# Optimization experiments

Hardware: AMD Instinct MI355X
Metric: run time of the kernel (lower is better)

Reference implementation:

```python
import jax, jax.numpy as jnp
import numpy as np

POOL = (2, 2)
B, H, W, C = 8, 128, 128, 256
FLAT_OUT = (H * POOL[0]) * (W * POOL[1]) * C  # 16,777,216


def setup_inputs() -> dict:
    key = jax.random.key(0)
    k1, k2 = jax.random.split(key)
    updates = jax.random.normal(k1, (B, H, W, C), dtype=jnp.float32)
    mask = jax.random.randint(k2, (B, H, W, C), 0, FLAT_OUT, dtype=jnp.int32)
    return {"updates": updates, "mask": mask}


def reference(updates, mask):
    ph, pw = POOL
    b, h, w, c = updates.shape
    hout, wout = h * ph, w * pw
    flat_input_size = h * w * c            # NOTE: original uses INPUT size as batch offset
    flat_output_size = hout * wout * c
    # per-batch offset (replicates b * flat_input_size from the TF code)
    batch_range = jnp.arange(b, dtype=jnp.int32).reshape(-1, 1, 1, 1)
    flat_mask = (mask.astype(jnp.int32) + batch_range * flat_input_size).reshape(-1)
    flat_updates = updates.reshape(-1)
    flat_output = jnp.zeros((b * flat_output_size,), dtype=updates.dtype)
    flat_output = flat_output.at[flat_mask].add(flat_updates)
    return flat_output.reshape(b, hout, wout, c)
```

## Files before the change

kernel.cpp:

```cpp
#include <hip/hip_runtime.h>


typedef float floatx4 __attribute__((ext_vector_type(4)));

constexpr int FLAT_IN   = 1 << 22;
constexpr int N_ELEMS   = 8 * FLAT_IN;
constexpr int OUT_WIN   = 7 * FLAT_IN + (1 << 24);
constexpr int OUT_TOTAL = 134217728;

constexpr int FB_SHIFT = 14;
constexpr int BKT_SIZE = 1 << FB_SHIFT;
constexpr int NBF      = OUT_WIN >> FB_SHIFT;
constexpr int CB_SHIFT = 16;
constexpr int NBC      = OUT_WIN >> CB_SHIFT;
constexpr int NBC_PAD  = 768;

constexpr int PBLOCK   = 1024;
constexpr int CHUNK    = 131072;
constexpr int NBLK     = N_ELEMS / CHUNK;
constexpr int ITERS    = CHUNK / (4 * PBLOCK);
constexpr int SEGS     = 8;
constexpr int SEG_ROWS = NBLK / SEGS;

constexpr size_t WS_PAIRS  = 0;
constexpr size_t WS_HISTC  = 268435456;
constexpr size_t WS_SEGC   = WS_HISTC + (size_t)NBLK * NBC_PAD * 4;
constexpr size_t WS_BBC    = WS_SEGC + (size_t)SEGS * NBC_PAD * 4;
constexpr size_t WS_FH     = WS_BBC + 3328;
constexpr size_t WS_BBF    = WS_FH + (size_t)NBF * 4;
constexpr size_t WS_NEEDED = WS_BBF + (size_t)(NBF + 1) * 4;

__global__ __launch_bounds__(256) void zero_kernel(floatx4* __restrict__ p, int n4) {
  int i = blockIdx.x * 256 + threadIdx.x;
  int stride = gridDim.x * 256;
  floatx4 z = {0.f, 0.f, 0.f, 0.f};
  for (; i < n4; i += stride) __builtin_nontemporal_store(z, p + i);
}

__global__ __launch_bounds__(PBLOCK) void p1_hist(const int4* __restrict__ mask4,
                                                  int* __restrict__ hist_c,
                                                  int* __restrict__ fhist) {
  __shared__ int cnt[1024];
  const int blk = blockIdx.x, tid = threadIdx.x;
  if (tid < 1024) cnt[tid] = 0;
  __syncthreads();
  const int base4 = blk * (CHUNK / 4);
  #pragma unroll 4
  for (int k = 0; k < ITERS; ++k) {
    int4 m = mask4[base4 + k * PBLOCK + tid];
    atomicAdd(&cnt[m.x >> FB_SHIFT], 1);
    atomicAdd(&cnt[m.y >> FB_SHIFT], 1);
    atomicAdd(&cnt[m.z >> FB_SHIFT], 1);
    atomicAdd(&cnt[m.w >> FB_SHIFT], 1);
  }
  __syncthreads();
  const int boff = (blk * CHUNK) & ~(FLAT_IN - 1);
  const int f0   = boff >> FB_SHIFT;
  const int cb0  = f0 >> 2;
  for (int j = tid; j < 1024; j += PBLOCK)
    if (cnt[j]) atomicAdd(&fhist[f0 + j], cnt[j]);
  for (int j = tid; j < NBC_PAD; j += PBLOCK) {
    int v = 0;
    int jj = j - cb0;
    if (jj >= 0 && jj < 256)
      v = cnt[4 * jj] + cnt[4 * jj + 1] + cnt[4 * jj + 2] + cnt[4 * jj + 3];
    hist_c[blk * NBC_PAD + j] = v;
  }
}

__global__ __launch_bounds__(256) void p2_segsum(const int* __restrict__ hist,
                                                 int* __restrict__ segsum) {
  int b = blockIdx.x * 256 + threadIdx.x;
  int seg = blockIdx.y;
  const int* p = hist + (size_t)(seg * SEG_ROWS) * NBC_PAD + b;
  int s = 0;
  #pragma unroll 4
  for (int k = 0; k < SEG_ROWS; ++k) s += p[(size_t)k * NBC_PAD];
  segsum[seg * NBC_PAD + b] = s;
}

__global__ __launch_bounds__(256) void p2_scan_c(const int* __restrict__ segsum,
                                                 int* __restrict__ bbase) {
  __shared__ int tot[NBC_PAD];
  __shared__ int partial[256];
  const int t = threadIdx.x;
  for (int j = t; j < NBC_PAD; j += 256) {
    int s = 0;
    #pragma unroll
    for (int g = 0; g < SEGS; ++g) s += segsum[g * NBC_PAD + j];
    tot[j] = s;
  }
  __syncthreads();
  int local = 0;
  #pragma unroll
  for (int k = 0; k < NBC_PAD / 256; ++k) local += tot[t * (NBC_PAD / 256) + k];
  partial[t] = local;
  __syncthreads();
  for (int off = 1; off < 256; off <<= 1) {
    int tmp = (t >= off) ? partial[t - off] : 0;
    __syncthreads();
    partial[t] += tmp;
    __syncthreads();
  }
  int run = partial[t] - local;
  #pragma unroll
  for (int k = 0; k < NBC_PAD / 256; ++k) {
    int b = t * (NBC_PAD / 256) + k;
    bbase[b] = run;
    run += tot[b];
  }
  if (t == 255) bbase[NBC_PAD] = run;
}

__global__ __launch_bounds__(256) void p2_expand(int* __restrict__ hist,
                                                 const int* __restrict__ segsum) {
  int b = blockIdx.x * 256 + threadIdx.x;
  int seg = blockIdx.y;
  int run = 0;
  for (int g = 0; g < seg; ++g) run += segsum[g * NBC_PAD + b];
  int* p = hist + (size_t)(seg * SEG_ROWS) * NBC_PAD + b;
  for (int k = 0; k < SEG_ROWS; ++k) {
    int v = p[(size_t)k * NBC_PAD];
    p[(size_t)k * NBC_PAD] = run;
    run += v;
  }
}

__global__ __launch_bounds__(256) void p2_scan_f(const int* __restrict__ fhist,
                                                 int* __restrict__ bbase) {
  __shared__ int tot[NBF];
  __shared__ int partial[256];
  const int t = threadIdx.x;
  for (int j = t; j < NBF; j += 256) tot[j] = fhist[j];
  __syncthreads();
  int local = 0;
  #pragma unroll
  for (int k = 0; k < NBF / 256; ++k) local += tot[t * (NBF / 256) + k];
  partial[t] = local;
  __syncthreads();
  for (int off = 1; off < 256; off <<= 1) {
    int tmp = (t >= off) ? partial[t - off] : 0;
    __syncthreads();
    partial[t] += tmp;
    __syncthreads();
  }
  int run = partial[t] - local;
  #pragma unroll
  for (int k = 0; k < NBF / 256; ++k) {
    int b = t * (NBF / 256) + k;
    bbase[b] = run;
    run += tot[b];
  }
  if (t == 255) bbase[NBF] = run;
}

__global__ __launch_bounds__(PBLOCK) void p3a_place(const int4* __restrict__ mask4,
                                                    const float4* __restrict__ upd4,
                                                    const int* __restrict__ hist_c,
                                                    const int* __restrict__ bbase_c,
                                                    int2* __restrict__ pout) {
  __shared__ int cnt[256];
  __shared__ int rowbase[256];
  const int blk = blockIdx.x, tid = threadIdx.x;
  const int boff = (blk * CHUNK) & ~(FLAT_IN - 1);
  const int cb0 = boff >> CB_SHIFT;
  if (tid < 256) {
    cnt[tid] = 0;
    rowbase[tid] = bbase_c[cb0 + tid] + hist_c[blk * NBC_PAD + cb0 + tid];
  }
  __syncthreads();
  const int base4 = blk * (CHUNK / 4);
  #pragma unroll 2
  for (int k = 0; k < ITERS; ++k) {
    int j4 = base4 + k * PBLOCK + tid;
    int4 m = mask4[j4];
    float4 u = upd4[j4];
    {
      int b = m.x >> CB_SHIFT; int r = atomicAdd(&cnt[b], 1);
      pout[rowbase[b] + r] = make_int2(m.x + boff, __float_as_int(u.x));
    }
    {
      int b = m.y >> CB_SHIFT; int r = atomicAdd(&cnt[b], 1);
      pout[rowbase[b] + r] = make_int2(m.y + boff, __float_as_int(u.y));
    }
    {
      int b = m.z >> CB_SHIFT; int r = atomicAdd(&cnt[b], 1);
      pout[rowbase[b] + r] = make_int2(m.z + boff, __float_as_int(u.z));
    }
    {
      int b = m.w >> CB_SHIFT; int r = atomicAdd(&cnt[b], 1);
      pout[rowbase[b] + r] = make_int2(m.w + boff, __float_as_int(u.w));
    }
  }
}

__device__ __forceinline__ void pushA(int idx, int val, int* cnt, const int* fb,
                                      int2* __restrict__ pout) {
  int f = (idx >> FB_SHIFT) & 3;
  unsigned long long act = __ballot(1);
  unsigned long long b0 = __ballot(f & 1);
  unsigned long long b1 = __ballot(f & 2);
  unsigned long long mf = ((f & 1) ? b0 : ~b0) & ((f & 2) ? b1 : ~b1) & act;
  int lane = threadIdx.x & 63;
  int rank = __popcll(mf & ((1ull << lane) - 1ull));
  int leader = __ffsll((unsigned long long)mf) - 1;
  int r0 = 0;
  if (lane == leader) r0 = atomicAdd(&cnt[f], __popcll(mf));
  r0 = __shfl(r0, leader);
  pout[fb[f] + r0 + rank] = make_int2(idx, val);
}

__global__ __launch_bounds__(512) void p3b_fine(const int2* __restrict__ pin,
                                                const int* __restrict__ bbase_c,
                                                const int* __restrict__ bbase_f,
                                                int2* __restrict__ pout) {
  __shared__ int cnt[4];
  __shared__ int fb[4];
  const int cb = blockIdx.x, tid = threadIdx.x;
  if (tid < 4) {
    cnt[tid] = 0;
    fb[tid] = bbase_f[cb * 4 + tid];
  }
  __syncthreads();
  const int s = bbase_c[cb], e = bbase_c[cb + 1];
  const int s4 = (s + 1) & ~1;
  if ((s & 1) && s < e && tid == 0) {
    int2 p = pin[s];
    int f = (p.x >> FB_SHIFT) & 3;
    int r = atomicAdd(&cnt[f], 1);
    pout[fb[f] + r] = p;
  }
  const int n2 = (e > s4) ? ((e - s4) >> 1) : 0;
  const int4* pv = (const int4*)(pin + s4);
  for (int i = tid; i < n2; i += 512) {
    int4 q = pv[i];
    pushA(q.x, q.y, cnt, fb, pout);
    pushA(q.z, q.w, cnt, fb, pout);
  }
  if ((e > s4) && ((e - s4) & 1) && tid == 0) {
    int2 p = pin[e - 1];
    int f = (p.x >> FB_SHIFT) & 3;
    int r = atomicAdd(&cnt[f], 1);
    pout[fb[f] + r] = p;
  }
}

__global__ __launch_bounds__(256) void p4_apply(const int2* __restrict__ pairs,
                                                const int* __restrict__ bbase,
                                                float* __restrict__ out) {
  __shared__ float win[BKT_SIZE];
  const int bkt = blockIdx.x, tid = threadIdx.x;
  floatx4* w4 = (floatx4*)win;
  floatx4 z = {0.f, 0.f, 0.f, 0.f};
  #pragma unroll
  for (int k = 0; k < BKT_SIZE / 1024; ++k) w4[k * 256 + tid] = z;
  __syncthreads();
  const int s = bbase[bkt], e = bbase[bkt + 1];
  const int s4 = (s + 1) & ~1;
  if ((s & 1) && s < e && tid == 0) {
    int2 p = pairs[s];
    atomicAdd(&win[p.x & (BKT_SIZE - 1)], __int_as_float(p.y));
  }
  const int n2 = (e > s4) ? ((e - s4) >> 1) : 0;
  const int4* pv = (const int4*)(pairs + s4);
  for (int i = tid; i < n2; i += 256) {
    int4 q = pv[i];
    atomicAdd(&win[q.x & (BKT_SIZE - 1)], __int_as_float(q.y));
    atomicAdd(&win[q.z & (BKT_SIZE - 1)], __int_as_float(q.w));
  }
  if ((e > s4) && ((e - s4) & 1) && tid == 0) {
    int2 p = pairs[e - 1];
    atomicAdd(&win[p.x & (BKT_SIZE - 1)], __int_as_float(p.y));
  }
  __syncthreads();
  floatx4* o4 = (floatx4*)(out + (size_t)bkt * BKT_SIZE);
  #pragma unroll
  for (int k = 0; k < BKT_SIZE / 1024; ++k)
    __builtin_nontemporal_store(w4[k * 256 + tid], o4 + k * 256 + tid);
}

__global__ __launch_bounds__(256) void scatter_add4_kernel(
    const float4* __restrict__ upd4, const int4* __restrict__ msk4,
    float* __restrict__ out, int n4) {
  int j = blockIdx.x * blockDim.x + threadIdx.x;
  if (j >= n4) return;
  float4 u = upd4[j];
  int4 m = msk4[j];
  int base = (j * 4) & ~(FLAT_IN - 1);
  unsafeAtomicAdd(out + (base + m.x), u.x);
  unsafeAtomicAdd(out + (base + m.y), u.y);
  unsafeAtomicAdd(out + (base + m.z), u.z);
  unsafeAtomicAdd(out + (base + m.w), u.w);
}

extern "C" void kernel_launch(void* const* d_in, const int* in_sizes, int n_in,
                              void* d_out, int out_size, void* d_ws, size_t ws_size,
                              hipStream_t stream) {
  const float* updates = (const float*)d_in[0];
  const int*   mask    = (const int*)d_in[1];
  float*       out     = (float*)d_out;
  const int n = in_sizes[0];

  const bool fast = (n == N_ELEMS) && (out_size == OUT_TOTAL) && (ws_size >= WS_NEEDED);

  if (!fast) {
    int n4z = out_size / 4;
    zero_kernel<<<(n4z + 2047) / 2048, 256, 0, stream>>>((floatx4*)d_out, n4z);
    int n4 = n / 4;
    scatter_add4_kernel<<<(n4 + 255) / 256, 256, 0, stream>>>(
        (const float4*)updates, (const int4*)mask, out, n4);
    return;
  }

  char* ws = (char*)d_ws;
  int2* pairs_f = (int2*)(ws + WS_PAIRS);
  int*  hist_c  = (int*)(ws + WS_HISTC);
  int*  segsum  = (int*)(ws + WS_SEGC);
  int*  bbase_c = (int*)(ws + WS_BBC);
  int*  fhist   = (int*)(ws + WS_FH);
  int*  bbase_f = (int*)(ws + WS_BBF);
  int2* pairs_c = (int2*)(out + OUT_WIN);

  zero_kernel<<<1, 256, 0, stream>>>((floatx4*)fhist, NBF / 4);
  p1_hist<<<NBLK, PBLOCK, 0, stream>>>((const int4*)mask, hist_c, fhist);
  p2_segsum<<<dim3(NBC_PAD / 256, SEGS), 256, 0, stream>>>(hist_c, segsum);
  p2_scan_c<<<1, 256, 0, stream>>>(segsum, bbase_c);
  p2_expand<<<dim3(NBC_PAD / 256, SEGS), 256, 0, stream>>>(hist_c, segsum);
  p2_scan_f<<<1, 256, 0, stream>>>(fhist, bbase_f);
  p3a_place<<<NBLK, PBLOCK, 0, stream>>>((const int4*)mask, (const float4*)updates,
                                         hist_c, bbase_c, pairs_c);
  p3b_fine<<<NBC, 512, 0, stream>>>(pairs_c, bbase_c, bbase_f, pairs_f);
  {
    int n4 = (OUT_TOTAL - OUT_WIN) / 4;
    zero_kernel<<<5376, 256, 0, stream>>>((floatx4*)(out + OUT_WIN), n4);
  }
  p4_apply<<<NBF, 256, 0, stream>>>(pairs_f, bbase_f, out);
}
```

Before: 1.219 ms.

## Drop fine bucketing pass; apply from coarse buckets with split 128KB LDS windows

Removes the fine histogram, its scan, and the second partitioning pass (p3b_fine) that re-sorted the pairs into 16K-element buckets. Pairs are now written once, into coarse 64K-element buckets in workspace. Each coarse bucket is then read by two blocks, and each block accumulates only the half that matches its selector bit into a 32K-float LDS window. The same apply kernel also zero-fills the output tail beyond the window, so the separate zero kernel goes away, and the block order is permuted. This saves one full read and write of the pair stream, at the cost of each coarse bucket's pairs being read twice and of larger 1024-thread blocks with 128KB of LDS, which may lower occupancy.

```diff
diff --git a/kernel.cpp b/kernel.cpp
--- a/kernel.cpp
+++ b/kernel.cpp
@@ -8,12 +8,14 @@
 constexpr int OUT_WIN   = 7 * FLAT_IN + (1 << 24);
 constexpr int OUT_TOTAL = 134217728;
 
-constexpr int FB_SHIFT = 14;
-constexpr int BKT_SIZE = 1 << FB_SHIFT;
-constexpr int NBF      = OUT_WIN >> FB_SHIFT;
 constexpr int CB_SHIFT = 16;
 constexpr int NBC      = OUT_WIN >> CB_SHIFT;
 constexpr int NBC_PAD  = 768;
+
+constexpr int AP_SHIFT = 15;
+constexpr int APW      = 1 << AP_SHIFT;
+constexpr int NAP      = OUT_TOTAL >> AP_SHIFT;
+constexpr int NAP_WIN  = OUT_WIN >> AP_SHIFT;
 
 constexpr int PBLOCK   = 1024;
 constexpr int CHUNK    = 131072;
@@ -26,9 +28,7 @@
 constexpr size_t WS_HISTC  = 268435456;
 constexpr size_t WS_SEGC   = WS_HISTC + (size_t)NBLK * NBC_PAD * 4;
 constexpr size_t WS_BBC    = WS_SEGC + (size_t)SEGS * NBC_PAD * 4;
-constexpr size_t WS_FH     = WS_BBC + 3328;
-constexpr size_t WS_BBF    = WS_FH + (size_t)NBF * 4;
-constexpr size_t WS_NEEDED = WS_BBF + (size_t)(NBF + 1) * 4;
+constexpr size_t WS_NEEDED = WS_BBC + (size_t)(NBC_PAD + 1) * 4;
 
 __global__ __launch_bounds__(256) void zero_kernel(floatx4* __restrict__ p, int n4) {
   int i = blockIdx.x * 256 + threadIdx.x;
@@ -38,33 +38,25 @@
 }
 
 __global__ __launch_bounds__(PBLOCK) void p1_hist(const int4* __restrict__ mask4,
-                                                  int* __restrict__ hist_c,
-                                                  int* __restrict__ fhist) {
-  __shared__ int cnt[1024];
+                                                  int* __restrict__ hist_c) {
+  __shared__ int cnt[256];
   const int blk = blockIdx.x, tid = threadIdx.x;
-  if (tid < 1024) cnt[tid] = 0;
+  if (tid < 256) cnt[tid] = 0;
   __syncthreads();
   const int base4 = blk * (CHUNK / 4);
   #pragma unroll 4
   for (int k = 0; k < ITERS; ++k) {
     int4 m = mask4[base4 + k * PBLOCK + tid];
-    atomicAdd(&cnt[m.x >> FB_SHIFT], 1);
-    atomicAdd(&cnt[m.y >> FB_SHIFT], 1);
-    atomicAdd(&cnt[m.z >> FB_SHIFT], 1);
-    atomicAdd(&cnt[m.w >> FB_SHIFT], 1);
-  }
-  __syncthreads();
-  const int boff = (blk * CHUNK) & ~(FLAT_IN - 1);
-  const int f0   = boff >> FB_SHIFT;
-  const int cb0  = f0 >> 2;
-  for (int j = tid; j < 1024; j += PBLOCK)
-    if (cnt[j]) atomicAdd(&fhist[f0 + j], cnt[j]);
+    atomicAdd(&cnt[m.x >> CB_SHIFT], 1);
+    atomicAdd(&cnt[m.y >> CB_SHIFT], 1);
+    atomicAdd(&cnt[m.z >> CB_SHIFT], 1);
+    atomicAdd(&cnt[m.w >> CB_SHIFT], 1);
+  }
+  __syncthreads();
+  const int cb0 = ((blk * CHUNK) & ~(FLAT_IN - 1)) >> CB_SHIFT;
   for (int j = tid; j < NBC_PAD; j += PBLOCK) {
-    int v = 0;
     int jj = j - cb0;
-    if (jj >= 0 && jj < 256)
-      v = cnt[4 * jj] + cnt[4 * jj + 1] + cnt[4 * jj + 2] + cnt[4 * jj + 3];
-    hist_c[blk * NBC_PAD + j] = v;
+    hist_c[blk * NBC_PAD + j] = (jj >= 0 && jj < 256) ? cnt[jj] : 0;
   }
 }
 
@@ -124,34 +116,6 @@
     p[(size_t)k * NBC_PAD] = run;
     run += v;
   }
-}
-
-__global__ __launch_bounds__(256) void p2_scan_f(const int* __restrict__ fhist,
-                                                 int* __restrict__ bbase) {
-  __shared__ int tot[NBF];
-  __shared__ int partial[256];
-  const int t = threadIdx.x;
-  for (int j = t; j < NBF; j += 256) tot[j] = fhist[j];
-  __syncthreads();
-  int local = 0;
-  #pragma unroll
-  for (int k = 0; k < NBF / 256; ++k) local += tot[t * (NBF / 256) + k];
-  partial[t] = local;
-  __syncthreads();
-  for (int off = 1; off < 256; off <<= 1) {
-    int tmp = (t >= off) ? partial[t - off] : 0;
-    __syncthreads();
-    partial[t] += tmp;
-    __syncthreads();
-  }
-  int run = partial[t] - local;
-  #pragma unroll
-  for (int k = 0; k < NBF / 256; ++k) {
-    int b = t * (NBF / 256) + k;
-    bbase[b] = run;
-    run += tot[b];
-  }
-  if (t == 255) bbase[NBF] = run;
 }
 
 __global__ __launch_bounds__(PBLOCK) void p3a_place(const int4* __restrict__ mask4,
@@ -194,89 +158,48 @@
   }
 }
 
-__device__ __forceinline__ void pushA(int idx, int val, int* cnt, const int* fb,
-                                      int2* __restrict__ pout) {
-  int f = (idx >> FB_SHIFT) & 3;
-  unsigned long long act = __ballot(1);
-  unsigned long long b0 = __ballot(f & 1);
-  unsigned long long b1 = __ballot(f & 2);
-  unsigned long long mf = ((f & 1) ? b0 : ~b0) & ((f & 2) ? b1 : ~b1) & act;
-  int lane = threadIdx.x & 63;
-  int rank = __popcll(mf & ((1ull << lane) - 1ull));
-  int leader = __ffsll((unsigned long long)mf) - 1;
-  int r0 = 0;
-  if (lane == leader) r0 = atomicAdd(&cnt[f], __popcll(mf));
-  r0 = __shfl(r0, leader);
-  pout[fb[f] + r0 + rank] = make_int2(idx, val);
-}
-
-__global__ __launch_bounds__(512) void p3b_fine(const int2* __restrict__ pin,
-                                                const int* __restrict__ bbase_c,
-                                                const int* __restrict__ bbase_f,
-                                                int2* __restrict__ pout) {
-  __shared__ int cnt[4];
-  __shared__ int fb[4];
-  const int cb = blockIdx.x, tid = threadIdx.x;
-  if (tid < 4) {
-    cnt[tid] = 0;
-    fb[tid] = bbase_f[cb * 4 + tid];
-  }
-  __syncthreads();
-  const int s = bbase_c[cb], e = bbase_c[cb + 1];
-  const int s4 = (s + 1) & ~1;
-  if ((s & 1) && s < e && tid == 0) {
-    int2 p = pin[s];
-    int f = (p.x >> FB_SHIFT) & 3;
-    int r = atomicAdd(&cnt[f], 1);
-    pout[fb[f] + r] = p;
-  }
-  const int n2 = (e > s4) ? ((e - s4) >> 1) : 0;
-  const int4* pv = (const int4*)(pin + s4);
-  for (int i = tid; i < n2; i += 512) {
-    int4 q = pv[i];
-    pushA(q.x, q.y, cnt, fb, pout);
-    pushA(q.z, q.w, cnt, fb, pout);
-  }
-  if ((e > s4) && ((e - s4) & 1) && tid == 0) {
-    int2 p = pin[e - 1];
-    int f = (p.x >> FB_SHIFT) & 3;
-    int r = atomicAdd(&cnt[f], 1);
-    pout[fb[f] + r] = p;
-  }
-}
-
-__global__ __launch_bounds__(256) void p4_apply(const int2* __restrict__ pairs,
-                                                const int* __restrict__ bbase,
-                                                float* __restrict__ out) {
-  __shared__ float win[BKT_SIZE];
-  const int bkt = blockIdx.x, tid = threadIdx.x;
+__global__ __launch_bounds__(1024) void p4c_apply(const int2* __restrict__ pairs,
+                                                  const int* __restrict__ bbase,
+                                                  float* __restrict__ out) {
+  __shared__ float win[APW];
+  const int tid = threadIdx.x;
+  const int b = blockIdx.x;
+  const int h = (b & ~15) | ((b & 7) << 1) | ((b >> 3) & 1);
   floatx4* w4 = (floatx4*)win;
   floatx4 z = {0.f, 0.f, 0.f, 0.f};
   #pragma unroll
-  for (int k = 0; k < BKT_SIZE / 1024; ++k) w4[k * 256 + tid] = z;
-  __syncthreads();
-  const int s = bbase[bkt], e = bbase[bkt + 1];
-  const int s4 = (s + 1) & ~1;
-  if ((s & 1) && s < e && tid == 0) {
-    int2 p = pairs[s];
-    atomicAdd(&win[p.x & (BKT_SIZE - 1)], __int_as_float(p.y));
-  }
-  const int n2 = (e > s4) ? ((e - s4) >> 1) : 0;
-  const int4* pv = (const int4*)(pairs + s4);
-  for (int i = tid; i < n2; i += 256) {
-    int4 q = pv[i];
-    atomicAdd(&win[q.x & (BKT_SIZE - 1)], __int_as_float(q.y));
-    atomicAdd(&win[q.z & (BKT_SIZE - 1)], __int_as_float(q.w));
-  }
-  if ((e > s4) && ((e - s4) & 1) && tid == 0) {
-    int2 p = pairs[e - 1];
-    atomicAdd(&win[p.x & (BKT_SIZE - 1)], __int_as_float(p.y));
-  }
-  __syncthreads();
-  floatx4* o4 = (floatx4*)(out + (size_t)bkt * BKT_SIZE);
-  #pragma unroll
-  for (int k = 0; k < BKT_SIZE / 1024; ++k)
-    __builtin_nontemporal_store(w4[k * 256 + tid], o4 + k * 256 + tid);
+  for (int k = 0; k < APW / 4096; ++k) w4[k * 1024 + tid] = z;
+  if (h < NAP_WIN) {
+    __syncthreads();
+    const int cb = h >> 1;
+    const int sel = h & 1;
+    const int s = bbase[cb], e = bbase[cb + 1];
+    const int s4 = (s + 1) & ~1;
+    if ((s & 1) && s < e && tid == 0) {
+      int2 p = pairs[s];
+      if (((p.x >> AP_SHIFT) & 1) == sel)
+        atomicAdd(&win[p.x & (APW - 1)], __int_as_float(p.y));
+    }
+    const int n2 = (e > s4) ? ((e - s4) >> 1) : 0;
+    const int4* pv = (const int4*)(pairs + s4);
+    for (int i = tid; i < n2; i += 1024) {
+      int4 q = pv[i];
+      if (((q.x >> AP_SHIFT) & 1) == sel)
+        atomicAdd(&win[q.x & (APW - 1)], __int_as_float(q.y));
+      if (((q.z >> AP_SHIFT) & 1) == sel)
+        atomicAdd(&win[q.z & (APW - 1)], __int_as_float(q.w));
+    }
+    if ((e > s4) && ((e - s4) & 1) && tid == 0) {
+      int2 p = pairs[e - 1];
+      if (((p.x >> AP_SHIFT) & 1) == sel)
+        atomicAdd(&win[p.x & (APW - 1)], __int_as_float(p.y));
+    }
+    __syncthreads();
+  }
+  floatx4* o4 = (floatx4*)(out + (size_t)h * APW);
+  #pragma unroll
+  for (int k = 0; k < APW / 4096; ++k)
+    __builtin_nontemporal_store(w4[k * 1024 + tid], o4 + k * 1024 + tid);
 }
 
 __global__ __launch_bounds__(256) void scatter_add4_kernel(
@@ -313,26 +236,16 @@
   }
 
   char* ws = (char*)d_ws;
-  int2* pairs_f = (int2*)(ws + WS_PAIRS);
+  int2* pairs   = (int2*)(ws + WS_PAIRS);
   int*  hist_c  = (int*)(ws + WS_HISTC);
   int*  segsum  = (int*)(ws + WS_SEGC);
   int*  bbase_c = (int*)(ws + WS_BBC);
-  int*  fhist   = (int*)(ws + WS_FH);
-  int*  bbase_f = (int*)(ws + WS_BBF);
-  int2* pairs_c = (int2*)(out + OUT_WIN);
-
-  zero_kernel<<<1, 256, 0, stream>>>((floatx4*)fhist, NBF / 4);
-  p1_hist<<<NBLK, PBLOCK, 0, stream>>>((const int4*)mask, hist_c, fhist);
+
+  p1_hist<<<NBLK, PBLOCK, 0, stream>>>((const int4*)mask, hist_c);
   p2_segsum<<<dim3(NBC_PAD / 256, SEGS), 256, 0, stream>>>(hist_c, segsum);
   p2_scan_c<<<1, 256, 0, stream>>>(segsum, bbase_c);
   p2_expand<<<dim3(NBC_PAD / 256, SEGS), 256, 0, stream>>>(hist_c, segsum);
-  p2_scan_f<<<1, 256, 0, stream>>>(fhist, bbase_f);
   p3a_place<<<NBLK, PBLOCK, 0, stream>>>((const int4*)mask, (const float4*)updates,
-                                         hist_c, bbase_c, pairs_c);
-  p3b_fine<<<NBC, 512, 0, stream>>>(pairs_c, bbase_c, bbase_f, pairs_f);
-  {
-    int n4 = (OUT_TOTAL - OUT_WIN) / 4;
-    zero_kernel<<<5376, 256, 0, stream>>>((floatx4*)(out + OUT_WIN), n4);
-  }
-  p4_apply<<<NBF, 256, 0, stream>>>(pairs_f, bbase_f, out);
-}
+                                         hist_c, bbase_c, pairs);
+  p4c_apply<<<NAP, 1024, 0, stream>>>(pairs, bbase_c, out);
+}
```

After: 1.109 ms. -9.0%, faster.
